# Kernel tuning notes

Measured on AMD Instinct MI355X. Metric: run time of the kernel, lower is better.

## Reference

```python
import jax, jax.numpy as jnp
import numpy as np

D_MODEL = 512
N_HEAD = 8
D_K = 64
D_V = 64
D_HID = 2048
N_LAYERS = 2
BATCH = 16384
SEQ = 8
N_AGENTS = 8  # agent_index = i % 8 in original Encoder.forward
LN_EPS = 1e-6


def sinusoid_table(n_pos, d):
    # matches PositionalEncoding._get_sinusoid_encoding_table
    pos = jnp.arange(n_pos, dtype=jnp.float32)[:, None]              # [P,1]
    j = jnp.arange(d, dtype=jnp.float32)[None, :]                     # [1,D]
    angle = pos / jnp.power(10000.0, 2.0 * jnp.floor(j / 2.0) / d)    # [P,D]
    even = jnp.sin(angle[:, 0::2])
    odd = jnp.cos(angle[:, 1::2])
    tab = jnp.zeros((n_pos, d), jnp.float32)
    tab = tab.at[:, 0::2].set(even).at[:, 1::2].set(odd)
    return tab


def layer_norm(x, g, b):
    mu = jnp.mean(x, axis=-1, keepdims=True)
    var = jnp.mean(jnp.square(x - mu), axis=-1, keepdims=True)
    return (x - mu) * jax.lax.rsqrt(var + LN_EPS) * g + b


def setup_inputs() -> dict:
    key = jax.random.key(0)
    ks = jax.random.split(key, 8)
    s_attn = 1.0 / np.sqrt(D_MODEL)
    s_ffn1 = 1.0 / np.sqrt(D_MODEL)
    s_ffn2 = 1.0 / np.sqrt(D_HID)
    L = N_LAYERS
    return {
        "x": jax.random.normal(ks[0], (BATCH, SEQ, D_MODEL), jnp.float32),
        "Wq": jax.random.normal(ks[1], (L, D_MODEL, N_HEAD * D_K), jnp.float32) * s_attn,
        "bq": jnp.zeros((L, N_HEAD * D_K), jnp.float32),
        "Wk": jax.random.normal(ks[2], (L, D_MODEL, N_HEAD * D_K), jnp.float32) * s_attn,
        "bk": jnp.zeros((L, N_HEAD * D_K), jnp.float32),
        "Wv": jax.random.normal(ks[3], (L, D_MODEL, N_HEAD * D_V), jnp.float32) * s_attn,
        "bv": jnp.zeros((L, N_HEAD * D_V), jnp.float32),
        "Wo": jax.random.normal(ks[4], (L, N_HEAD * D_V, D_MODEL), jnp.float32) * s_attn,
        "bo": jnp.zeros((L, D_MODEL), jnp.float32),
        "ln1_g": jnp.ones((L, D_MODEL), jnp.float32),
        "ln1_b": jnp.zeros((L, D_MODEL), jnp.float32),
        "W1": jax.random.normal(ks[5], (L, D_MODEL, D_HID), jnp.float32) * s_ffn1,
        "b1": jnp.zeros((L, D_HID), jnp.float32),
        "W2": jax.random.normal(ks[6], (L, D_HID, D_MODEL), jnp.float32) * s_ffn2,
        "b2": jnp.zeros((L, D_MODEL), jnp.float32),
        "ln2_g": jnp.ones((L, D_MODEL), jnp.float32),
        "ln2_b": jnp.zeros((L, D_MODEL), jnp.float32),
    }


def reference(x, Wq, bq, Wk, bk, Wv, bv, Wo, bo, ln1_g, ln1_b,
              W1, b1, W2, b2, ln2_g, ln2_b):
    B, S, D = x.shape
    # positional encoding add (PositionalEncoding.forward)
    h = x + sinusoid_table(S, D)[None, :, :]
    scale = 1.0 / np.sqrt(D_K)
    for l in range(N_LAYERS):
        # --- multi-head self attention (post-LN residual) ---
        q = (h @ Wq[l] + bq[l]).reshape(B, S, N_HEAD, D_K)
        k = (h @ Wk[l] + bk[l]).reshape(B, S, N_HEAD, D_K)
        v = (h @ Wv[l] + bv[l]).reshape(B, S, N_HEAD, D_V)
        scores = jnp.einsum("bqhd,bkhd->bhqk", q, k) * scale
        attn = jax.nn.softmax(scores, axis=-1)
        ctx = jnp.einsum("bhqk,bkhd->bqhd", attn, v).reshape(B, S, N_HEAD * D_V)
        h = layer_norm(ctx @ Wo[l] + bo[l] + h, ln1_g[l], ln1_b[l])
        # --- position-wise FFN (post-LN residual) ---
        ffn = jax.nn.relu(h @ W1[l] + b1[l]) @ W2[l] + b2[l]
        h = layer_norm(ffn + h, ln2_g[l], ln2_b[l])
    # enc_out[i] = enc_input[i % 8]  (vectorized agent-token gather)
    idx = jnp.arange(B) % N_AGENTS
    return h[jnp.arange(B), idx]  # [B, D_MODEL]
```

## Files before the change

### kernel.cpp

```cpp
#include <hip/hip_runtime.h>

typedef unsigned short u16;
typedef unsigned int u32;
typedef __attribute__((ext_vector_type(8))) unsigned short u16x8;
typedef __attribute__((ext_vector_type(4))) float f32x4;

#define NTOK 131072
#define NSEL 16384

__device__ __forceinline__ float b2f(u16 v) {
  return __uint_as_float(((u32)v) << 16);
}
__device__ __forceinline__ u16 f2b(float f) {
  u32 u = __float_as_uint(f);
  u32 r = u + 0x7fffu + ((u >> 16) & 1u);
  return (u16)(r >> 16);
}

__device__ __forceinline__ void gload16(const void* g, void* l) {
  __builtin_amdgcn_global_load_lds((const __attribute__((address_space(1))) void*)g,
                                   (__attribute__((address_space(3))) void*)l, 16, 0, 0);
}

__device__ __forceinline__ void mfma16(f32x4& c, u16x8 a, u16x8 b) {
  asm("v_mfma_f32_16x16x32_bf16 %0, %1, %2, %0" : "+v"(c) : "v"(a), "v"(b));
}

#define BAR() __builtin_amdgcn_s_barrier()
#define VM(n) asm volatile("s_waitcnt vmcnt(" #n ")" ::: "memory")
#define PRIO1() __builtin_amdgcn_s_setprio(1)
#define PRIO0() __builtin_amdgcn_s_setprio(0)

__global__ __launch_bounds__(256) void table_kernel(float* __restrict__ tab) {
  const int i = blockIdx.x * 256 + threadIdx.x;
  if (i >= 4096) return;
  const int p = i >> 9, j = i & 511;
  const float ex = 2.f * (float)(j >> 1) / 512.f;
  const float ang = (float)p * powf(10000.f, -ex);
  tab[i] = (j & 1) ? cosf(ang) : sinf(ang);
}

__global__ __launch_bounds__(256) void biaspack_kernel(const float* __restrict__ bq,
                                                       const float* __restrict__ bk,
                                                       const float* __restrict__ bv,
                                                       float* __restrict__ dst) {
  const int i = blockIdx.x * 256 + threadIdx.x;
  if (i >= 3072) return;
  const int l = i / 1536, j = i % 1536;
  float v;
  if (j < 512) v = bq[l * 512 + j];
  else if (j < 1024) v = bk[l * 512 + j - 512];
  else v = bv[l * 512 + j - 1024];
  dst[i] = v;
}

struct TJob { const float* src; u16* dst; int Ki, Ni, blk0; };
struct TJobs { TJob j[12]; };

__global__ __launch_bounds__(256) void wconv_kernel(TJobs jobs) {
  __shared__ float tile[64][65];
  const int bid = blockIdx.x;
  int ji = 0;
#pragma unroll
  for (int t = 1; t < 12; ++t)
    if (bid >= jobs.j[t].blk0) ji = t;
  const TJob J = jobs.j[ji];
  const int rel = bid - J.blk0;
  const int ntn = J.Ni >> 6;
  const int tk = rel / ntn, tn = rel % ntn;
  const int tid = threadIdx.x;
  const int cn = tid & 63, rk = tid >> 6;
#pragma unroll
  for (int r = 0; r < 16; ++r) {
    const int kk = rk + r * 4;
    tile[kk][cn] = J.src[(size_t)(tk * 64 + kk) * J.Ni + tn * 64 + cn];
  }
  __syncthreads();
  const int ck = tid & 63, rn = tid >> 6;
#pragma unroll
  for (int r = 0; r < 16; ++r) {
    const int nn = rn + r * 4;
    J.dst[(size_t)(tn * 64 + nn) * J.Ki + tk * 64 + ck] = f2b(tile[ck][nn]);
  }
}

__global__ __launch_bounds__(256) void posenc_kernel(const float* __restrict__ x,
                                                     const float* __restrict__ tab,
                                                     u16* __restrict__ h) {
  const int i = blockIdx.x * 256 + threadIdx.x;
  const size_t e0 = (size_t)i * 8;
  const int d = (int)(e0 & 511);
  const int srow = (int)((e0 >> 9) & 7);
  const float4 a0 = *(const float4*)(x + e0);
  const float4 a1 = *(const float4*)(x + e0 + 4);
  const float* tp = tab + srow * 512 + d;
  float v[8] = {a0.x, a0.y, a0.z, a0.w, a1.x, a1.y, a1.z, a1.w};
  u16x8 o;
#pragma unroll
  for (int e = 0; e < 8; ++e) o[e] = f2b(v[e] + tp[e]);
  *(u16x8*)(h + e0) = o;
}

#define RDA(c, mh)                                                                  \
  A0 = *(const u16x8*)&As[c][wrbase + ((((mh) << 6) + 0 + lr) << 6) + swk0];        \
  A1 = *(const u16x8*)&As[c][wrbase + ((((mh) << 6) + 0 + lr) << 6) + swk1];        \
  A2 = *(const u16x8*)&As[c][wrbase + ((((mh) << 6) + 16 + lr) << 6) + swk0];       \
  A3 = *(const u16x8*)&As[c][wrbase + ((((mh) << 6) + 16 + lr) << 6) + swk1];       \
  A4 = *(const u16x8*)&As[c][wrbase + ((((mh) << 6) + 32 + lr) << 6) + swk0];       \
  A5 = *(const u16x8*)&As[c][wrbase + ((((mh) << 6) + 32 + lr) << 6) + swk1];       \
  A6 = *(const u16x8*)&As[c][wrbase + ((((mh) << 6) + 48 + lr) << 6) + swk0];       \
  A7 = *(const u16x8*)&As[c][wrbase + ((((mh) << 6) + 48 + lr) << 6) + swk1]

#define RDB(c, nh, V00, V01, V10, V11)                                                   \
  V00 = *(const u16x8*)&Bs[c][wcbase + ((brow0 + (((nh) << 1) + 0) * 16 + lr) << 6) + swk0]; \
  V01 = *(const u16x8*)&Bs[c][wcbase + ((brow0 + (((nh) << 1) + 0) * 16 + lr) << 6) + swk1]; \
  V10 = *(const u16x8*)&Bs[c][wcbase + ((brow0 + (((nh) << 1) + 1) * 16 + lr) << 6) + swk0]; \
  V11 = *(const u16x8*)&Bs[c][wcbase + ((brow0 + (((nh) << 1) + 1) * 16 + lr) << 6) + swk1]

#define QM(mh, nh, V00, V01, V10, V11)                \
  mfma16(acc[((mh) << 2) + 0][((nh) << 1) + 0], A0, V00); \
  mfma16(acc[((mh) << 2) + 0][((nh) << 1) + 1], A0, V10); \
  mfma16(acc[((mh) << 2) + 1][((nh) << 1) + 0], A2, V00); \
  mfma16(acc[((mh) << 2) + 1][((nh) << 1) + 1], A2, V10); \
  mfma16(acc[((mh) << 2) + 2][((nh) << 1) + 0], A4, V00); \
  mfma16(acc[((mh) << 2) + 2][((nh) << 1) + 1], A4, V10); \
  mfma16(acc[((mh) << 2) + 3][((nh) << 1) + 0], A6, V00); \
  mfma16(acc[((mh) << 2) + 3][((nh) << 1) + 1], A6, V10); \
  mfma16(acc[((mh) << 2) + 0][((nh) << 1) + 0], A1, V01); \
  mfma16(acc[((mh) << 2) + 0][((nh) << 1) + 1], A1, V11); \
  mfma16(acc[((mh) << 2) + 1][((nh) << 1) + 0], A3, V01); \
  mfma16(acc[((mh) << 2) + 1][((nh) << 1) + 1], A3, V11); \
  mfma16(acc[((mh) << 2) + 2][((nh) << 1) + 0], A5, V01); \
  mfma16(acc[((mh) << 2) + 2][((nh) << 1) + 1], A5, V11); \
  mfma16(acc[((mh) << 2) + 3][((nh) << 1) + 0], A7, V01); \
  mfma16(acc[((mh) << 2) + 3][((nh) << 1) + 1], A7, V11)

template <int RELU>
__global__ __launch_bounds__(512, 1) void gemm256(const u16* __restrict__ A,
                                                  const u16* __restrict__ Bt,
                                                  const float* __restrict__ bias,
                                                  u16* __restrict__ C, int M, int N, int K) {
  __shared__ __align__(16) u16 As[2][16384];
  __shared__ __align__(16) u16 Bs[2][16384];
  const int nbn = N >> 8;
  const int cpx = gridDim.x >> 3;
  const int bid = blockIdx.x;
  const int wgid = (bid & 7) * cpx + (bid >> 3);
  const int bm = wgid / nbn, bn = wgid - bm * nbn;
  const int tid = threadIdx.x;
  const int wid = tid >> 6, lane = tid & 63;
  const int wr = wid >> 2, wc = wid & 3;
  const int lr = lane & 15, kg0 = lane >> 4;
  const int swk0 = ((kg0 ^ (lr & 7)) << 3);
  const int swk1 = (((kg0 + 4) ^ (lr & 7)) << 3);
  const int wrbase = wr << 13;
  const int wcbase = (wc >> 1) << 13;
  const int brow0 = (wc & 1) << 6;
  const int rowinc = tid >> 3;
  const int gcol = (((tid & 7) ^ (rowinc & 7)) << 3);
  const u16* Ag = A + (size_t)((bm << 8) + rowinc) * K + gcol;
  const u16* Bg = Bt + (size_t)((bn << 8) + rowinc) * K + gcol;
  const int ldsw = wid << 9;

  f32x4 acc[8][4];
  const f32x4 zero = {0.f, 0.f, 0.f, 0.f};
#pragma unroll
  for (int m = 0; m < 8; ++m)
#pragma unroll
    for (int n = 0; n < 4; ++n) acc[m][n] = zero;

  u16x8 A0, A1, A2, A3, A4, A5, A6, A7;
  u16x8 B00, B01, B10, B11;
  u16x8 C00, C01, C10, C11;

  auto stgA = [&](int c, int h, int koff) {
    gload16(Ag + (size_t)(h << 7) * K + koff, &As[c][(h << 13) + ldsw]);
    gload16(Ag + (size_t)((h << 7) + 64) * K + koff, &As[c][(h << 13) + 4096 + ldsw]);
  };
  auto stgB = [&](int c, int h, int koff) {
    gload16(Bg + (size_t)(h << 7) * K + koff, &Bs[c][(h << 13) + ldsw]);
    gload16(Bg + (size_t)((h << 7) + 64) * K + koff, &Bs[c][(h << 13) + 4096 + ldsw]);
  };

  stgA(0, 0, 0); stgA(0, 1, 0); stgB(0, 0, 0); stgB(0, 1, 0);
  stgB(1, 0, 64); stgB(1, 1, 64);
  VM(4);
  BAR();

  const int niter = K >> 7;
  int k1 = 64, k2 = 128, k3 = 192;
#pragma unroll 1
  for (int i = 0; i < niter - 1; ++i) {
    RDA(0, 0); RDB(0, 0, B00, B01, B10, B11); stgA(1, 0, k1);
    PRIO1(); QM(0, 0, B00, B01, B10, B11); PRIO0();
    RDB(0, 1, C00, C01, C10, C11); stgA(1, 1, k1);
    PRIO1(); QM(0, 1, C00, C01, C10, C11); PRIO0(); BAR();
    RDA(0, 1); stgB(0, 0, k2);
    PRIO1(); QM(1, 1, C00, C01, C10, C11); PRIO0();
    stgB(0, 1, k2);
    PRIO1(); QM(1, 0, B00, B01, B10, B11); PRIO0(); VM(4); BAR();
    RDA(1, 0); RDB(1, 0, B00, B01, B10, B11); stgA(0, 0, k2);
    PRIO1(); QM(0, 0, B00, B01, B10, B11); PRIO0();
    RDB(1, 1, C00, C01, C10, C11); stgA(0, 1, k2);
    PRIO1(); QM(0, 1, C00, C01, C10, C11); PRIO0(); BAR();
    RDA(1, 1); stgB(1, 0, k3);
    PRIO1(); QM(1, 1, C00, C01, C10, C11); PRIO0();
    stgB(1, 1, k3);
    PRIO1(); QM(1, 0, B00, B01, B10, B11); PRIO0(); VM(4); BAR();
    k1 += 128; k2 += 128; k3 += 128;
  }
  RDA(0, 0); RDB(0, 0, B00, B01, B10, B11); stgA(1, 0, k1);
  PRIO1(); QM(0, 0, B00, B01, B10, B11); PRIO0();
  RDB(0, 1, C00, C01, C10, C11); stgA(1, 1, k1);
  PRIO1(); QM(0, 1, C00, C01, C10, C11); PRIO0(); BAR();
  RDA(0, 1);
  PRIO1(); QM(1, 1, C00, C01, C10, C11); PRIO0();
  PRIO1(); QM(1, 0, B00, B01, B10, B11); PRIO0(); VM(0); BAR();
  RDA(1, 0); RDB(1, 0, B00, B01, B10, B11);
  PRIO1(); QM(0, 0, B00, B01, B10, B11); PRIO0();
  RDB(1, 1, C00, C01, C10, C11);
  PRIO1(); QM(0, 1, C00, C01, C10, C11); PRIO0(); BAR();
  RDA(1, 1);
  PRIO1(); QM(1, 1, C00, C01, C10, C11); PRIO0();
  PRIO1(); QM(1, 0, B00, B01, B10, B11); PRIO0();

  const int r0 = kg0 << 2;
  const int cc = lr;
#pragma unroll
  for (int m8 = 0; m8 < 8; ++m8) {
    const size_t grow = (size_t)((bm << 8) + (wr << 7) + (m8 << 4) + r0);
#pragma unroll
    for (int n4 = 0; n4 < 4; ++n4) {
      const int gc = (bn << 8) + (wc << 6) + (n4 << 4) + cc;
      const float bv = bias[gc];
#pragma unroll
      for (int rr = 0; rr < 4; ++rr) {
        float v = acc[m8][n4][rr] + bv;
        if (RELU) v = fmaxf(v, 0.f);
        C[(grow + rr) * (size_t)N + gc] = f2b(v);
      }
    }
  }
}

__global__ __launch_bounds__(256) void attn_kernel(const u16* __restrict__ QKV,
                                                   u16* __restrict__ ctx) {
  __shared__ __align__(16) u16 sm[4][3][8][72];
  __shared__ float at[4][8][8];
  const int tid = threadIdx.x;
  const int wid = tid >> 6, lane = tid & 63;
  const int bh = blockIdx.x * 4 + wid;
  const int b = bh >> 3, h = bh & 7;
  const int s = lane >> 3, g = lane & 7;
  const u16* base = QKV + (size_t)(b * 8 + s) * 1536 + h * 64 + g * 8;
#pragma unroll
  for (int t = 0; t < 3; ++t)
    *(u16x8*)&sm[wid][t][s][g * 8] = *(const u16x8*)(base + t * 512);
  __syncthreads();
  float sc = 0.f;
#pragma unroll
  for (int c = 0; c < 8; ++c) {
    const int cg = ((c + g) & 7) * 8;
    u16x8 qv = *(const u16x8*)&sm[wid][0][s][cg];
    u16x8 kv = *(const u16x8*)&sm[wid][1][g][cg];
#pragma unroll
    for (int e = 0; e < 8; ++e) sc += b2f(qv[e]) * b2f(kv[e]);
  }
  sc *= 0.125f;
  float mx = fmaxf(sc, __shfl_xor(sc, 1));
  mx = fmaxf(mx, __shfl_xor(mx, 2));
  mx = fmaxf(mx, __shfl_xor(mx, 4));
  const float ex = __expf(sc - mx);
  float sum = ex;
  sum += __shfl_xor(sum, 1);
  sum += __shfl_xor(sum, 2);
  sum += __shfl_xor(sum, 4);
  at[wid][s][g] = ex / sum;
  __syncthreads();
  float o[8] = {0.f, 0.f, 0.f, 0.f, 0.f, 0.f, 0.f, 0.f};
#pragma unroll
  for (int j = 0; j < 8; ++j) {
    const float a = at[wid][s][j];
    u16x8 vv = *(const u16x8*)&sm[wid][2][j][g * 8];
#pragma unroll
    for (int e = 0; e < 8; ++e) o[e] += a * b2f(vv[e]);
  }
  u16x8 ov;
#pragma unroll
  for (int e = 0; e < 8; ++e) ov[e] = f2b(o[e]);
  *(u16x8*)(ctx + (size_t)(b * 8 + s) * 512 + h * 64 + g * 8) = ov;
}

__global__ __launch_bounds__(256) void attn_sel_kernel(const u16* __restrict__ KV,
                                                       const u16* __restrict__ Qs,
                                                       u16* __restrict__ ctx) {
  __shared__ __align__(16) u16 sm[4][2][8][72];
  __shared__ float at[4][8];
  const int tid = threadIdx.x;
  const int wid = tid >> 6, lane = tid & 63;
  const int bh = blockIdx.x * 4 + wid;
  const int b = bh >> 3, h = bh & 7;
  const int s = lane >> 3, g = lane & 7;
  const u16* base = KV + (size_t)(b * 8 + s) * 1024 + h * 64 + g * 8;
  *(u16x8*)&sm[wid][0][s][g * 8] = *(const u16x8*)(base);
  *(u16x8*)&sm[wid][1][s][g * 8] = *(const u16x8*)(base + 512);
  const u16x8 qv = *(const u16x8*)(Qs + (size_t)b * 512 + h * 64 + g * 8);
  __syncthreads();
  float p = 0.f;
  {
    u16x8 kv8 = *(const u16x8*)&sm[wid][0][s][g * 8];
#pragma unroll
    for (int e = 0; e < 8; ++e) p += b2f(qv[e]) * b2f(kv8[e]);
  }
  p += __shfl_xor(p, 1);
  p += __shfl_xor(p, 2);
  p += __shfl_xor(p, 4);
  p *= 0.125f;
  float mx = fmaxf(p, __shfl_xor(p, 8));
  mx = fmaxf(mx, __shfl_xor(mx, 16));
  mx = fmaxf(mx, __shfl_xor(mx, 32));
  const float ex = __expf(p - mx);
  float sum = ex;
  sum += __shfl_xor(sum, 8);
  sum += __shfl_xor(sum, 16);
  sum += __shfl_xor(sum, 32);
  if (g == 0) at[wid][s] = ex / sum;
  __syncthreads();
  if (s == 0) {
    float o[8] = {0.f, 0.f, 0.f, 0.f, 0.f, 0.f, 0.f, 0.f};
#pragma unroll
    for (int j = 0; j < 8; ++j) {
      const float a = at[wid][j];
      u16x8 vv = *(const u16x8*)&sm[wid][1][j][g * 8];
#pragma unroll
      for (int e = 0; e < 8; ++e) o[e] += a * b2f(vv[e]);
    }
    u16x8 ov;
#pragma unroll
    for (int e = 0; e < 8; ++e) ov[e] = f2b(o[e]);
    *(u16x8*)(ctx + (size_t)b * 512 + h * 64 + g * 8) = ov;
  }
}

template <int GATHER>
__global__ __launch_bounds__(256) void ln_kernel(const u16* __restrict__ t,
                                                 u16* __restrict__ h,
                                                 const float* __restrict__ gam,
                                                 const float* __restrict__ bet,
                                                 u16* __restrict__ hgat) {
  const int tid = threadIdx.x;
  const int wid = tid >> 6, lane = tid & 63;
  const int row = blockIdx.x * 4 + wid;
  const size_t base = (size_t)row * 512 + lane * 8;
  u16x8 tv = *(const u16x8*)(t + base);
  u16x8 hv = *(const u16x8*)(h + base);
  float x[8];
  float s1 = 0.f, s2 = 0.f;
#pragma unroll
  for (int e = 0; e < 8; ++e) {
    x[e] = b2f(tv[e]) + b2f(hv[e]);
    s1 += x[e];
    s2 += x[e] * x[e];
  }
#pragma unroll
  for (int m = 1; m < 64; m <<= 1) {
    s1 += __shfl_xor(s1, m);
    s2 += __shfl_xor(s2, m);
  }
  const float mu = s1 * (1.f / 512.f);
  const float var = s2 * (1.f / 512.f) - mu * mu;
  const float rs = rsqrtf(var + 1e-6f);
  const float4 g0 = *(const float4*)(gam + lane * 8);
  const float4 g1 = *(const float4*)(gam + lane * 8 + 4);
  const float4 b0 = *(const float4*)(bet + lane * 8);
  const float4 b1 = *(const float4*)(bet + lane * 8 + 4);
  const float gv[8] = {g0.x, g0.y, g0.z, g0.w, g1.x, g1.y, g1.z, g1.w};
  const float bv[8] = {b0.x, b0.y, b0.z, b0.w, b1.x, b1.y, b1.z, b1.w};
  u16x8 yv;
#pragma unroll
  for (int e = 0; e < 8; ++e) yv[e] = f2b((x[e] - mu) * rs * gv[e] + bv[e]);
  *(u16x8*)(h + base) = yv;
  if (GATHER) {
    const int bb = row >> 3;
    if ((row & 7) == (bb & 7))
      *(u16x8*)(hgat + (size_t)bb * 512 + lane * 8) = yv;
  }
}

__global__ __launch_bounds__(256) void ln_gather_kernel(const u16* __restrict__ t,
                                                        const u16* __restrict__ h,
                                                        u16* __restrict__ hsel,
                                                        const float* __restrict__ gam,
                                                        const float* __restrict__ bet) {
  const int tid = threadIdx.x;
  const int wid = tid >> 6, lane = tid & 63;
  const int b = blockIdx.x * 4 + wid;
  const size_t tb = (size_t)(b * 8 + (b & 7));
  u16x8 tv = *(const u16x8*)(t + (size_t)b * 512 + lane * 8);
  u16x8 hv = *(const u16x8*)(h + tb * 512 + lane * 8);
  float x[8];
  float s1 = 0.f, s2 = 0.f;
#pragma unroll
  for (int e = 0; e < 8; ++e) {
    x[e] = b2f(tv[e]) + b2f(hv[e]);
    s1 += x[e];
    s2 += x[e] * x[e];
  }
#pragma unroll
  for (int m = 1; m < 64; m <<= 1) {
    s1 += __shfl_xor(s1, m);
    s2 += __shfl_xor(s2, m);
  }
  const float mu = s1 * (1.f / 512.f);
  const float var = s2 * (1.f / 512.f) - mu * mu;
  const float rs = rsqrtf(var + 1e-6f);
  const float4 g0 = *(const float4*)(gam + lane * 8);
  const float4 g1 = *(const float4*)(gam + lane * 8 + 4);
  const float4 b0 = *(const float4*)(bet + lane * 8);
  const float4 b1 = *(const float4*)(bet + lane * 8 + 4);
  const float gv[8] = {g0.x, g0.y, g0.z, g0.w, g1.x, g1.y, g1.z, g1.w};
  const float bv[8] = {b0.x, b0.y, b0.z, b0.w, b1.x, b1.y, b1.z, b1.w};
  u16x8 yv;
#pragma unroll
  for (int e = 0; e < 8; ++e) yv[e] = f2b((x[e] - mu) * rs * gv[e] + bv[e]);
  *(u16x8*)(hsel + (size_t)b * 512 + lane * 8) = yv;
}

__global__ __launch_bounds__(256) void ln_final_kernel(const u16* __restrict__ t,
                                                       const u16* __restrict__ hsel,
                                                       const float* __restrict__ gam,
                                                       const float* __restrict__ bet,
                                                       float* __restrict__ out) {
  const int tid = threadIdx.x;
  const int wid = tid >> 6, lane = tid & 63;
  const int b = blockIdx.x * 4 + wid;
  const size_t base = (size_t)b * 512 + lane * 8;
  u16x8 tv = *(const u16x8*)(t + base);
  u16x8 hv = *(const u16x8*)(hsel + base);
  float x[8];
  float s1 = 0.f, s2 = 0.f;
#pragma unroll
  for (int e = 0; e < 8; ++e) {
    x[e] = b2f(tv[e]) + b2f(hv[e]);
    s1 += x[e];
    s2 += x[e] * x[e];
  }
#pragma unroll
  for (int m = 1; m < 64; m <<= 1) {
    s1 += __shfl_xor(s1, m);
    s2 += __shfl_xor(s2, m);
  }
  const float mu = s1 * (1.f / 512.f);
  const float var = s2 * (1.f / 512.f) - mu * mu;
  const float rs = rsqrtf(var + 1e-6f);
  const float4 g0 = *(const float4*)(gam + lane * 8);
  const float4 g1 = *(const float4*)(gam + lane * 8 + 4);
  const float4 b0 = *(const float4*)(bet + lane * 8);
  const float4 b1 = *(const float4*)(bet + lane * 8 + 4);
  const float gv[8] = {g0.x, g0.y, g0.z, g0.w, g1.x, g1.y, g1.z, g1.w};
  const float bv[8] = {b0.x, b0.y, b0.z, b0.w, b1.x, b1.y, b1.z, b1.w};
  float y[8];
#pragma unroll
  for (int e = 0; e < 8; ++e) y[e] = (x[e] - mu) * rs * gv[e] + bv[e];
  float4* op = (float4*)(out + base);
  op[0] = make_float4(y[0], y[1], y[2], y[3]);
  op[1] = make_float4(y[4], y[5], y[6], y[7]);
}

static void launch_gemm(const u16* A, const u16* Bt, const float* bias, u16* C, int M, int N,
                        int K, int relu, hipStream_t st) {
  dim3 grid((M >> 8) * (N >> 8));
  if (relu)
    gemm256<1><<<grid, 512, 0, st>>>(A, Bt, bias, C, M, N, K);
  else
    gemm256<0><<<grid, 512, 0, st>>>(A, Bt, bias, C, M, N, K);
}

extern "C" void kernel_launch(void* const* d_in, const int* in_sizes, int n_in, void* d_out,
                              int out_size, void* d_ws, size_t ws_size, hipStream_t stream) {
  const float* x = (const float*)d_in[0];
  const float* Wq = (const float*)d_in[1];
  const float* bq = (const float*)d_in[2];
  const float* Wk = (const float*)d_in[3];
  const float* bk = (const float*)d_in[4];
  const float* Wv = (const float*)d_in[5];
  const float* bv = (const float*)d_in[6];
  const float* Wo = (const float*)d_in[7];
  const float* bo = (const float*)d_in[8];
  const float* ln1g = (const float*)d_in[9];
  const float* ln1b = (const float*)d_in[10];
  const float* W1 = (const float*)d_in[11];
  const float* b1 = (const float*)d_in[12];
  const float* W2 = (const float*)d_in[13];
  const float* b2 = (const float*)d_in[14];
  const float* ln2g = (const float*)d_in[15];
  const float* ln2b = (const float*)d_in[16];
  float* out = (float*)d_out;

  char* ws = (char*)d_ws;
  const size_t o_tab = 0;
  const size_t o_bqkv = 16384;
  const size_t o_w = 28672;
  const size_t o_h = o_w + 12582912;
  const size_t o_buf = o_h + (size_t)NTOK * 512 * 2;
  const size_t o_tmp = o_buf + (size_t)NTOK * 2048 * 2;
  const size_t o_hsel = o_tmp + (size_t)NTOK * 512 * 2;
  const size_t o_hgat = o_hsel + (size_t)NSEL * 512 * 2;
  const size_t need = o_hgat + (size_t)NSEL * 512 * 2;
  if (ws_size < need) return;

  float* tab = (float*)(ws + o_tab);
  float* bqkv = (float*)(ws + o_bqkv);
  u16* wbf = (u16*)(ws + o_w);
  u16* h = (u16*)(ws + o_h);
  u16* buf = (u16*)(ws + o_buf);
  u16* ctx = buf + (size_t)NTOK * 1536;
  u16* tmp = (u16*)(ws + o_tmp);
  u16* hsel = (u16*)(ws + o_hsel);
  u16* hgat = (u16*)(ws + o_hgat);

  table_kernel<<<16, 256, 0, stream>>>(tab);
  biaspack_kernel<<<12, 256, 0, stream>>>(bq, bk, bv, bqkv);

  TJobs jobs;
  int blk = 0, nj = 0;
  auto add = [&](const float* s, u16* dmat, int Ki, int Ni) {
    jobs.j[nj].src = s;
    jobs.j[nj].dst = dmat;
    jobs.j[nj].Ki = Ki;
    jobs.j[nj].Ni = Ni;
    jobs.j[nj].blk0 = blk;
    ++nj;
    blk += (Ki / 64) * (Ni / 64);
  };
  for (int l = 0; l < 2; ++l) {
    u16* wl = wbf + (size_t)l * 3145728;
    add(Wq + (size_t)l * 262144, wl, 512, 512);
    add(Wk + (size_t)l * 262144, wl + 262144, 512, 512);
    add(Wv + (size_t)l * 262144, wl + 524288, 512, 512);
    add(Wo + (size_t)l * 262144, wl + 786432, 512, 512);
    add(W1 + (size_t)l * 1048576, wl + 1048576, 512, 2048);
    add(W2 + (size_t)l * 1048576, wl + 2097152, 2048, 512);
  }
  wconv_kernel<<<blk, 256, 0, stream>>>(jobs);
  posenc_kernel<<<32768, 256, 0, stream>>>(x, tab, h);

  {
    u16* wl = wbf;
    launch_gemm(h, wl, bqkv, buf, NTOK, 1536, 512, 0, stream);
    attn_kernel<<<32768, 256, 0, stream>>>(buf, ctx);
    launch_gemm(ctx, wl + 786432, bo, tmp, NTOK, 512, 512, 0, stream);
    ln_kernel<0><<<32768, 256, 0, stream>>>(tmp, h, ln1g, ln1b, nullptr);
    launch_gemm(h, wl + 1048576, b1, buf, NTOK, 2048, 512, 1, stream);
    launch_gemm(buf, wl + 2097152, b2, tmp, NTOK, 512, 2048, 0, stream);
    ln_kernel<1><<<32768, 256, 0, stream>>>(tmp, h, ln2g, ln2b, hgat);
  }

  {
    u16* wl = wbf + 3145728;
    u16* kv = buf;
    u16* qsel = buf + (size_t)NTOK * 1024;
    u16* ctx_sel = qsel + (size_t)NSEL * 512;
    u16* hid_sel = ctx_sel + (size_t)NSEL * 512;
    u16* tmp_sel = tmp;
    launch_gemm(h, wl + 262144, bqkv + 1536 + 512, kv, NTOK, 1024, 512, 0, stream);
    launch_gemm(hgat, wl, bqkv + 1536, qsel, NSEL, 512, 512, 0, stream);
    attn_sel_kernel<<<32768, 256, 0, stream>>>(kv, qsel, ctx_sel);
    launch_gemm(ctx_sel, wl + 786432, bo + 512, tmp_sel, NSEL, 512, 512, 0, stream);
    ln_gather_kernel<<<NSEL / 4, 256, 0, stream>>>(tmp_sel, h, hsel, ln1g + 512, ln1b + 512);
    launch_gemm(hsel, wl + 1048576, b1 + 2048, hid_sel, NSEL, 2048, 512, 1, stream);
    launch_gemm(hid_sel, wl + 2097152, b2 + 512, tmp_sel, NSEL, 512, 2048, 0, stream);
    ln_final_kernel<<<NSEL / 4, 256, 0, stream>>>(tmp_sel, hsel, ln2g + 512, ln2b + 512, out);
  }
}
```

Measured before the change: 1.636 ms.

## Add 128x128 triple-buffered GEMM kernel for large FFN and KV projections

Adds a new GEMM kernel with 128x128 tiles, 256 threads, a three-stage LDS ring buffer loaded via global_load_lds with swizzled layout, and an XCD-aware block remapping. Uses it for the layer-1 FFN GEMMs and the layer-2 KV projection in place of the 256x256 kernel. The aim is higher occupancy (three blocks per CU) and deeper prefetch to better hide memory latency, at the cost of less operand reuse per tile and more global traffic.

```diff
diff --git a/kernel.cpp b/kernel.cpp
--- a/kernel.cpp
+++ b/kernel.cpp
@@ -243,6 +243,110 @@
   }
 }
 
+#define RD32(c)                                                      \
+  a0 = *(const u16x8*)&As3[c][((arow + 0 + lr) << 5) + swk];         \
+  a1 = *(const u16x8*)&As3[c][((arow + 16 + lr) << 5) + swk];        \
+  a2 = *(const u16x8*)&As3[c][((arow + 32 + lr) << 5) + swk];        \
+  a3 = *(const u16x8*)&As3[c][((arow + 48 + lr) << 5) + swk];        \
+  b0 = *(const u16x8*)&Bs3[c][((brow + 0 + lr) << 5) + swk];         \
+  b1 = *(const u16x8*)&Bs3[c][((brow + 16 + lr) << 5) + swk];        \
+  b2 = *(const u16x8*)&Bs3[c][((brow + 32 + lr) << 5) + swk];        \
+  b3 = *(const u16x8*)&Bs3[c][((brow + 48 + lr) << 5) + swk]
+
+#define MM32()                                                       \
+  mfma16(acc[0][0], a0, b0); mfma16(acc[0][1], a0, b1);              \
+  mfma16(acc[0][2], a0, b2); mfma16(acc[0][3], a0, b3);              \
+  mfma16(acc[1][0], a1, b0); mfma16(acc[1][1], a1, b1);              \
+  mfma16(acc[1][2], a1, b2); mfma16(acc[1][3], a1, b3);              \
+  mfma16(acc[2][0], a2, b0); mfma16(acc[2][1], a2, b1);              \
+  mfma16(acc[2][2], a2, b2); mfma16(acc[2][3], a2, b3);              \
+  mfma16(acc[3][0], a3, b0); mfma16(acc[3][1], a3, b1);              \
+  mfma16(acc[3][2], a3, b2); mfma16(acc[3][3], a3, b3)
+
+template <int RELU>
+__global__ __launch_bounds__(256, 3) void gemm128(const u16* __restrict__ A,
+                                                  const u16* __restrict__ Bt,
+                                                  const float* __restrict__ bias,
+                                                  u16* __restrict__ C, int M, int N, int K) {
+  __shared__ __align__(16) u16 As3[3][4096];
+  __shared__ __align__(16) u16 Bs3[3][4096];
+  const int nbn = N >> 7;
+  const int cpx = gridDim.x >> 3;
+  const int bid = blockIdx.x;
+  const int wgid = (bid & 7) * cpx + (bid >> 3);
+  const int bm = wgid / nbn, bn = wgid - bm * nbn;
+  const int tid = threadIdx.x;
+  const int wid = tid >> 6, lane = tid & 63;
+  const int wr = wid >> 1, wc = wid & 1;
+  const int lr = lane & 15, kg0 = lane >> 4;
+  const int swk = ((kg0 ^ ((lr >> 1) & 3)) << 3);
+  const int arow = wr << 6;
+  const int brow = wc << 6;
+  const int srow = tid >> 2;
+  const int scol = (((tid & 3) ^ ((tid >> 3) & 3)) << 3);
+  const u16* Ag = A + (size_t)((bm << 7) + srow) * K + scol;
+  const u16* Bg = Bt + (size_t)((bn << 7) + srow) * K + scol;
+
+  f32x4 acc[4][4];
+  const f32x4 zero = {0.f, 0.f, 0.f, 0.f};
+#pragma unroll
+  for (int m = 0; m < 4; ++m)
+#pragma unroll
+    for (int n = 0; n < 4; ++n) acc[m][n] = zero;
+
+  u16x8 a0, a1, a2, a3, b0, b1, b2, b3;
+
+  auto stg = [&](int c, int koff) {
+    gload16(Ag + koff, &As3[c][tid << 3]);
+    gload16(Ag + (size_t)64 * K + koff, &As3[c][2048 + (tid << 3)]);
+    gload16(Bg + koff, &Bs3[c][tid << 3]);
+    gload16(Bg + (size_t)64 * K + koff, &Bs3[c][2048 + (tid << 3)]);
+  };
+
+  stg(0, 0);
+  stg(1, 32);
+  VM(4);
+  BAR();
+
+  const int niter = K >> 5;
+  int c0 = 0, c2 = 2, koff = 64;
+#pragma unroll 1
+  for (int t = 0; t < niter - 2; ++t) {
+    RD32(c0);
+    stg(c2, koff);
+    PRIO1(); MM32(); PRIO0();
+    VM(4);
+    BAR();
+    c0 = (c0 == 2) ? 0 : c0 + 1;
+    c2 = (c2 == 2) ? 0 : c2 + 1;
+    koff += 32;
+  }
+  RD32(c0);
+  PRIO1(); MM32(); PRIO0();
+  VM(0);
+  BAR();
+  c0 = (c0 == 2) ? 0 : c0 + 1;
+  RD32(c0);
+  PRIO1(); MM32(); PRIO0();
+
+  const int r0 = kg0 << 2;
+#pragma unroll
+  for (int m = 0; m < 4; ++m) {
+    const size_t grow = (size_t)((bm << 7) + (wr << 6) + (m << 4) + r0);
+#pragma unroll
+    for (int n = 0; n < 4; ++n) {
+      const int gc = (bn << 7) + (wc << 6) + (n << 4) + lr;
+      const float bv = bias[gc];
+#pragma unroll
+      for (int rr = 0; rr < 4; ++rr) {
+        float v = acc[m][n][rr] + bv;
+        if (RELU) v = fmaxf(v, 0.f);
+        C[(grow + rr) * (size_t)N + gc] = f2b(v);
+      }
+    }
+  }
+}
+
 __global__ __launch_bounds__(256) void attn_kernel(const u16* __restrict__ QKV,
                                                    u16* __restrict__ ctx) {
   __shared__ __align__(16) u16 sm[4][3][8][72];
@@ -474,6 +578,15 @@
     gemm256<1><<<grid, 512, 0, st>>>(A, Bt, bias, C, M, N, K);
   else
     gemm256<0><<<grid, 512, 0, st>>>(A, Bt, bias, C, M, N, K);
+}
+
+static void launch_gemm128(const u16* A, const u16* Bt, const float* bias, u16* C, int M, int N,
+                           int K, int relu, hipStream_t st) {
+  dim3 grid((M >> 7) * (N >> 7));
+  if (relu)
+    gemm128<1><<<grid, 256, 0, st>>>(A, Bt, bias, C, M, N, K);
+  else
+    gemm128<0><<<grid, 256, 0, st>>>(A, Bt, bias, C, M, N, K);
 }
 
 extern "C" void kernel_launch(void* const* d_in, const int* in_sizes, int n_in, void* d_out,
@@ -551,8 +664,8 @@
     attn_kernel<<<32768, 256, 0, stream>>>(buf, ctx);
     launch_gemm(ctx, wl + 786432, bo, tmp, NTOK, 512, 512, 0, stream);
     ln_kernel<0><<<32768, 256, 0, stream>>>(tmp, h, ln1g, ln1b, nullptr);
-    launch_gemm(h, wl + 1048576, b1, buf, NTOK, 2048, 512, 1, stream);
-    launch_gemm(buf, wl + 2097152, b2, tmp, NTOK, 512, 2048, 0, stream);
+    launch_gemm128(h, wl + 1048576, b1, buf, NTOK, 2048, 512, 1, stream);
+    launch_gemm128(buf, wl + 2097152, b2, tmp, NTOK, 512, 2048, 0, stream);
     ln_kernel<1><<<32768, 256, 0, stream>>>(tmp, h, ln2g, ln2b, hgat);
   }
 
@@ -563,7 +676,7 @@
     u16* ctx_sel = qsel + (size_t)NSEL * 512;
     u16* hid_sel = ctx_sel + (size_t)NSEL * 512;
     u16* tmp_sel = tmp;
-    launch_gemm(h, wl + 262144, bqkv + 1536 + 512, kv, NTOK, 1024, 512, 0, stream);
+    launch_gemm128(h, wl + 262144, bqkv + 1536 + 512, kv, NTOK, 1024, 512, 0, stream);
     launch_gemm(hgat, wl, bqkv + 1536, qsel, NSEL, 512, 512, 0, stream);
     attn_sel_kernel<<<32768, 256, 0, stream>>>(kv, qsel, ctx_sel);
     launch_gemm(ctx_sel, wl + 786432, bo + 512, tmp_sel, NSEL, 512, 512, 0, stream);
```

Result: slower. 1.794 ms (+9.6%).
